# Kernel optimization log

Measured on AMD Instinct MI355X. Metric: run time of the kernel, lower is better.

The kernel has to match this reference:

```python
import jax, jax.numpy as jnp
import numpy as np

BQ, BK = 128, 64  # SpargeAttn-style Q/K block sizes
NEG = -1e30


def _block_mask(q, k, simthreshd1, cdfthreshd, scale):
    """Mean-similarity block selection: a (q-block, k-block) pair is pruned only
    when both blocks are self-similar (mean cosine sim to block mean exceeds the
    per-head simthreshd1) AND it is not in the top-CDF mass (cdfthreshd) of the
    compressed block-level softmax."""
    B, H, L, D = q.shape
    nq, nk = L // BQ, L // BK
    qb = q.reshape(B, H, nq, BQ, D)
    kb = k.reshape(B, H, nk, BK, D)
    qm = qb.mean(3)  # [B,H,nq,D] block means
    km = kb.mean(3)  # [B,H,nk,D]

    def blocksim(xb, xm):
        xn = xb / (jnp.linalg.norm(xb, axis=-1, keepdims=True) + 1e-6)
        mn = xm / (jnp.linalg.norm(xm, axis=-1, keepdims=True) + 1e-6)
        return jnp.einsum('bhntd,bhnd->bhnt', xn, mn).mean(-1)  # [B,H,n]

    th = simthreshd1[None, :, None]
    comp_q = blocksim(qb, qm) > th  # [B,H,nq] self-similar q blocks
    comp_k = blocksim(kb, km) > th  # [B,H,nk]

    # compressed attention over block means, then CDF-based top-mass selection
    p = jax.nn.softmax(jnp.einsum('bhqd,bhkd->bhqk', qm, km) * scale, axis=-1)
    order = jnp.argsort(-p, axis=-1)
    sp = jnp.take_along_axis(p, order, axis=-1)
    csum = jnp.cumsum(sp, axis=-1)
    keep_sorted = (csum - sp) < cdfthreshd[None, :, None, None]  # prefix covering tau
    rank = jnp.argsort(order, axis=-1)  # inverse permutation
    selected = jnp.take_along_axis(keep_sorted, rank, axis=-1)  # [B,H,nq,nk]

    return selected | ~(comp_q[..., :, None] & comp_k[..., None, :])


def setup_inputs() -> dict:
    key = jax.random.key(0)
    kq, kk, kv, kc = jax.random.split(key, 4)
    B, H, L, D = 1, 16, 2048, 64
    return {
        'q': jax.random.normal(kq, (B, H, L, D), dtype=jnp.float32),
        'k': jax.random.normal(kk, (B, H, L, D), dtype=jnp.float32),
        'v': jax.random.normal(kv, (B, H, L, D), dtype=jnp.float32),
        'simthreshd1': jnp.zeros((H,), dtype=jnp.float32),
        'cdfthreshd': jax.random.uniform(kc, (H,), dtype=jnp.float32),
    }


def reference(q, k, v, simthreshd1, cdfthreshd):
    B, H, L, D = q.shape
    scale = 1.0 / np.sqrt(D).astype(np.float32)
    # smooth_k: subtract per-(B,H) key mean (softmax-invariant shift, matches kernel)
    k = k - k.mean(axis=-2, keepdims=True)
    bmask = _block_mask(q, k, simthreshd1, cdfthreshd, scale)  # [B,H,nq,nk] bool
    mask_tok = jnp.repeat(jnp.repeat(bmask, BQ, axis=2), BK, axis=3)  # [B,H,L,L]
    s = jnp.einsum('bhqd,bhkd->bhqk', q, k) * scale
    s = jnp.where(mask_tok, s, NEG)
    p = jax.nn.softmax(s, axis=-1)
    return jnp.einsum('bhqk,bhkd->bhqd', p, v)
```

## Files before the change

### kernel.cpp

```cpp
#include <hip/hip_runtime.h>

#define HH 16
#define LL 2048
#define DD 64
#define BQ 128
#define BK 64
#define NQ (LL/BQ)
#define NK (LL/BK)
#define SCALE 0.125f
#define QSCALE (0.125f * 1.44269504f)

typedef __attribute__((ext_vector_type(8))) short s8v;
typedef __attribute__((ext_vector_type(4))) float f4v;

static __device__ __forceinline__ ushort f2bf(float x) {
    unsigned u = __float_as_uint(x);
    u += 0x7fff + ((u >> 16) & 1);
    return (ushort)(u >> 16);
}

__global__ void kmean1_kernel(const float* __restrict__ k, float* __restrict__ kpart) {
    int b = blockIdx.x;
    int h = blockIdx.y;
    int t = threadIdx.x;
    int d = t & 63, c = t >> 6;
    const float* kh = k + ((size_t)h*LL + (size_t)b*256) * DD;
    float s = 0.f;
    for (int l = c*64; l < c*64 + 64; ++l) s += kh[(size_t)l * DD + d];
    __shared__ float red[4][64];
    red[c][d] = s;
    __syncthreads();
    if (t < 64) kpart[((size_t)h*8 + b)*64 + t] = red[0][t]+red[1][t]+red[2][t]+red[3][t];
}

__global__ __launch_bounds__(128) void stats_kernel(
        const float* __restrict__ q, const float* __restrict__ k, const float* __restrict__ v,
        const float* __restrict__ kpart, const float* __restrict__ simth,
        float* __restrict__ qm, float* __restrict__ km,
        int* __restrict__ compq, int* __restrict__ compk,
        ushort* __restrict__ qb, ushort* __restrict__ kb, ushort* __restrict__ vTb) {
    __shared__ __align__(16) char smem[34304];
    int h = blockIdx.y, t = threadIdx.x;

    if ((int)blockIdx.x < NQ) {
        int qi = blockIdx.x;
        float (*xs)[DD+1] = (float(*)[DD+1])smem;
        float* mean = (float*)(smem + 33280);
        float* red  = (float*)(smem + 33536);
        size_t row = (size_t)h*LL + (size_t)qi*BQ + t;
        const float* rp = q + row * DD;
        float x[DD]; float n2 = 0.f;
        #pragma unroll
        for (int d = 0; d < DD; d += 4) {
            float4 v4 = *(const float4*)(rp + d);
            x[d]=v4.x; x[d+1]=v4.y; x[d+2]=v4.z; x[d+3]=v4.w;
            n2 += v4.x*v4.x + v4.y*v4.y + v4.z*v4.z + v4.w*v4.w;
        }
        #pragma unroll
        for (int d = 0; d < DD; d += 4) {
            ushort4 o;
            o.x = f2bf(x[d]*QSCALE);   o.y = f2bf(x[d+1]*QSCALE);
            o.z = f2bf(x[d+2]*QSCALE); o.w = f2bf(x[d+3]*QSCALE);
            *(ushort4*)(qb + row*DD + d) = o;
        }
        #pragma unroll
        for (int d = 0; d < DD; ++d) xs[t][d] = x[d];
        __syncthreads();
        {
            int d = t & 63, hf = t >> 6;
            float s = 0.f;
            for (int r = hf*64; r < hf*64 + 64; ++r) s += xs[r][d];
            red[t] = s;
        }
        __syncthreads();
        if (t < DD) mean[t] = (red[t] + red[64 + t]) * (1.0f/BQ);
        __syncthreads();
        float dot = 0.f, m2 = 0.f;
        #pragma unroll
        for (int d = 0; d < DD; ++d) { dot += x[d]*mean[d]; m2 += mean[d]*mean[d]; }
        float cs = dot / ((sqrtf(n2) + 1e-6f) * (sqrtf(m2) + 1e-6f));
        __syncthreads();
        red[t] = cs; __syncthreads();
        for (int sft = BQ/2; sft > 0; sft >>= 1) {
            if (t < sft) red[t] += red[t + sft];
            __syncthreads();
        }
        if (t == 0) compq[h*NQ + qi] = (red[0] * (1.0f/BQ)) > simth[h] ? 1 : 0;
        if (t < DD) qm[((size_t)h*NQ + qi)*DD + t] = mean[t];
    } else {
        int ki = blockIdx.x - NQ;
        float* mu_s = (float*)smem;
        float (*xs)[DD+1] = (float(*)[DD+1])(smem + 256);
        ushort (*vs)[66]  = (ushort(*)[66])(smem + 256 + 16640);
        float* mean = (float*)(smem + 256 + 16640 + 8448);
        float* red  = (float*)(smem + 256 + 16640 + 8448 + 256);
        if (t < 64) {
            float s = 0.f;
            #pragma unroll
            for (int b = 0; b < 8; ++b) s += kpart[((size_t)h*8 + b)*64 + t];
            mu_s[t] = s * (1.0f/LL);
        }
        __syncthreads();
        size_t rowb = (size_t)h*LL + (size_t)ki*BK;
        float x[DD]; float n2 = 0.f;
        if (t < 64) {
            const float* rp = k + (rowb + t) * DD;
            #pragma unroll
            for (int d = 0; d < DD; d += 4) {
                float4 v4 = *(const float4*)(rp + d);
                v4.x -= mu_s[d]; v4.y -= mu_s[d+1]; v4.z -= mu_s[d+2]; v4.w -= mu_s[d+3];
                x[d]=v4.x; x[d+1]=v4.y; x[d+2]=v4.z; x[d+3]=v4.w;
                n2 += v4.x*v4.x + v4.y*v4.y + v4.z*v4.z + v4.w*v4.w;
            }
            #pragma unroll
            for (int d = 0; d < DD; d += 4) {
                ushort4 o;
                o.x = f2bf(x[d]);   o.y = f2bf(x[d+1]);
                o.z = f2bf(x[d+2]); o.w = f2bf(x[d+3]);
                *(ushort4*)(kb + (rowb + t)*DD + d) = o;
            }
            #pragma unroll
            for (int d = 0; d < DD; ++d) xs[t][d] = x[d];
        } else {
            int tk = t - 64;
            const float* vp = v + (rowb + tk) * DD;
            #pragma unroll
            for (int d = 0; d < DD; d += 4) {
                float4 v4 = *(const float4*)(vp + d);
                vs[tk][d]   = f2bf(v4.x); vs[tk][d+1] = f2bf(v4.y);
                vs[tk][d+2] = f2bf(v4.z); vs[tk][d+3] = f2bf(v4.w);
            }
        }
        __syncthreads();
        if (t < 64) {
            size_t vbase = ((size_t)h*DD + t)*LL + (size_t)ki*64;
            #pragma unroll
            for (int r8 = 0; r8 < 64; r8 += 8) {
                s8v o;
                #pragma unroll
                for (int e = 0; e < 8; ++e) o[e] = (short)vs[r8+e][t];
                *(s8v*)(vTb + vbase + r8) = o;
            }
            float s = 0.f;
            for (int r = 0; r < BK; ++r) s += xs[r][t];
            mean[t] = s * (1.0f/BK);
        }
        __syncthreads();
        if (t < 64) {
            float dot = 0.f, m2 = 0.f;
            #pragma unroll
            for (int d = 0; d < DD; ++d) { dot += x[d]*mean[d]; m2 += mean[d]*mean[d]; }
            float cs = dot / ((sqrtf(n2) + 1e-6f) * (sqrtf(m2) + 1e-6f));
            red[t] = cs;
        }
        __syncthreads();
        for (int sft = 32; sft > 0; sft >>= 1) {
            if (t < sft) red[t] += red[t + sft];
            __syncthreads();
        }
        if (t == 0) compk[h*NK + ki] = (red[0] * (1.0f/BK)) > simth[h] ? 1 : 0;
        if (t < 64) km[((size_t)h*NK + ki)*DD + t] = mean[t];
    }
}

__global__ __launch_bounds__(256, 2) void attn_kernel(
        const ushort* __restrict__ qb, const ushort* __restrict__ kb,
        const ushort* __restrict__ vTb,
        const float* __restrict__ qm, const float* __restrict__ km,
        const int* __restrict__ compq, const int* __restrict__ compk,
        const float* __restrict__ cdfth, float* __restrict__ out) {
    __shared__ __align__(16) char shmem[69632];
    ushort* pl = (ushort*)shmem + (threadIdx.x >> 6) * 64 * 72;
    float*  Ob = (float*)shmem;
    float*  mb = (float*)(shmem + 67584);
    float*  lb = (float*)(shmem + 68608);

    int bid  = blockIdx.x;
    int slot = bid >> 3;
    int h    = ((slot >> 5) << 3) | (bid & 7);
    int qi   = (slot & 31) >> 1;
    int half = slot & 1;
    int tid  = threadIdx.x;
    int w    = tid >> 6;
    int l    = tid & 63;
    int lo = l & 15, hi = l >> 4;
    int r0 = qi*BQ + half*64;

    unsigned msk;
    {
        int j = l & 31;
        const float* qv = qm + ((size_t)h*NQ + qi)*DD;
        const float* kv = km + ((size_t)h*NK + j)*DD;
        float s = 0.f;
        #pragma unroll
        for (int d = 0; d < DD; d += 4) {
            float4 a = *(const float4*)(qv + d);
            float4 b = *(const float4*)(kv + d);
            s += a.x*b.x; s += a.y*b.y; s += a.z*b.z; s += a.w*b.w;
        }
        s *= SCALE;
        float mx = s;
        #pragma unroll
        for (int xm = 1; xm <= 16; xm <<= 1) mx = fmaxf(mx, __shfl_xor(mx, xm, 32));
        float e = expf(s - mx);
        float den = 0.f;
        for (int i = 0; i < 32; ++i) den += __shfl(e, i, 32);
        float p = e / den;
        float mass = 0.f;
        for (int i = 0; i < 32; ++i) {
            float pi = __shfl(p, i, 32);
            if (pi > p || (pi == p && i < j)) mass += pi;
        }
        int keep = (mass < cdfth[h]) || !(compq[h*NQ+qi] && compk[h*NK+j]);
        unsigned long long bal = __ballot(keep != 0);
        msk = (unsigned)bal;
    }

    const ushort* qh = qb  + (size_t)h*LL*DD;
    const ushort* kh = kb  + (size_t)h*LL*DD;
    const ushort* vh = vTb + (size_t)h*DD*LL;

    s8v qf[4][2];
    #pragma unroll
    for (int qt = 0; qt < 4; ++qt)
        #pragma unroll
        for (int kk = 0; kk < 2; ++kk)
            qf[qt][kk] = *(const s8v*)(qh + (size_t)(r0 + qt*16 + lo)*DD + kk*32 + hi*8);

    f4v O[4][4];
    float m[4], lsum[4];
    #pragma unroll
    for (int qt = 0; qt < 4; ++qt) {
        m[qt] = -1e30f; lsum[qt] = 0.f;
        #pragma unroll
        for (int dt = 0; dt < 4; ++dt) O[qt][dt] = (f4v){0.f,0.f,0.f,0.f};
    }

    unsigned mm = msk; int rank = 0;
    while (mm) {
        int j = __ffs(mm) - 1; mm &= mm - 1;
        if (((rank++) & 3) != w) continue;

        const ushort* kbj = kh + (size_t)j*BK*DD;
        const ushort* vbj = vh + (size_t)j*BK;

        s8v kf[4][2];
        #pragma unroll
        for (int kt = 0; kt < 4; ++kt)
            #pragma unroll
            for (int kk = 0; kk < 2; ++kk)
                kf[kt][kk] = *(const s8v*)(kbj + (size_t)(kt*16 + lo)*DD + kk*32 + hi*8);

        f4v S[4][4];
        #pragma unroll
        for (int kt = 0; kt < 4; ++kt)
            #pragma unroll
            for (int qt = 0; qt < 4; ++qt)
                S[kt][qt] = (f4v){0.f,0.f,0.f,0.f};
        __builtin_amdgcn_s_setprio(1);
        #pragma unroll
        for (int kk = 0; kk < 2; ++kk)
            #pragma unroll
            for (int kt = 0; kt < 4; ++kt)
                #pragma unroll
                for (int qt = 0; qt < 4; ++qt)
                    S[kt][qt] = __builtin_amdgcn_mfma_f32_16x16x32_bf16(kf[kt][kk], qf[qt][kk], S[kt][qt], 0, 0, 0);
        __builtin_amdgcn_s_setprio(0);

        s8v vf[2][4];
        #pragma unroll
        for (int kk = 0; kk < 2; ++kk)
            #pragma unroll
            for (int dt = 0; dt < 4; ++dt)
                vf[kk][dt] = *(const s8v*)(vbj + (size_t)(dt*16 + lo)*LL + kk*32 + hi*8);

        float pm[4];
        #pragma unroll
        for (int qt = 0; qt < 4; ++qt) {
            float a0 = fmaxf(fmaxf(S[0][qt][0],S[0][qt][1]), fmaxf(S[0][qt][2],S[0][qt][3]));
            float a1 = fmaxf(fmaxf(S[1][qt][0],S[1][qt][1]), fmaxf(S[1][qt][2],S[1][qt][3]));
            float a2 = fmaxf(fmaxf(S[2][qt][0],S[2][qt][1]), fmaxf(S[2][qt][2],S[2][qt][3]));
            float a3 = fmaxf(fmaxf(S[3][qt][0],S[3][qt][1]), fmaxf(S[3][qt][2],S[3][qt][3]));
            float p = fmaxf(fmaxf(a0,a1), fmaxf(a2,a3));
            p = fmaxf(p, __shfl_xor(p, 16));
            p = fmaxf(p, __shfl_xor(p, 32));
            pm[qt] = p;
        }
        bool grow = (pm[0] > m[0]+8.0f) | (pm[1] > m[1]+8.0f) |
                    (pm[2] > m[2]+8.0f) | (pm[3] > m[3]+8.0f);
        if (__any(grow)) {
            float alpha[4];
            #pragma unroll
            for (int qt = 0; qt < 4; ++qt) {
                float mn = fmaxf(m[qt], pm[qt]);
                alpha[qt] = __builtin_amdgcn_exp2f(m[qt] - mn);
                lsum[qt] *= alpha[qt];
                m[qt] = mn;
            }
            #pragma unroll
            for (int qt = 0; qt < 4; ++qt)
                #pragma unroll
                for (int r = 0; r < 4; ++r) {
                    float a = __shfl(alpha[qt], hi*4 + r);
                    #pragma unroll
                    for (int dt = 0; dt < 4; ++dt) O[qt][dt][r] *= a;
                }
        }
        #pragma unroll
        for (int qt = 0; qt < 4; ++qt) {
            float ps = 0.f;
            #pragma unroll
            for (int kt = 0; kt < 4; ++kt) {
                float p0 = __builtin_amdgcn_exp2f(S[kt][qt][0] - m[qt]);
                float p1 = __builtin_amdgcn_exp2f(S[kt][qt][1] - m[qt]);
                float p2 = __builtin_amdgcn_exp2f(S[kt][qt][2] - m[qt]);
                float p3 = __builtin_amdgcn_exp2f(S[kt][qt][3] - m[qt]);
                ps += (p0 + p1) + (p2 + p3);
                unsigned c01, c23;
                asm("v_cvt_pk_bf16_f32 %0, %1, %2" : "=v"(c01) : "v"(p0), "v"(p1));
                asm("v_cvt_pk_bf16_f32 %0, %1, %2" : "=v"(c23) : "v"(p2), "v"(p3));
                *(uint2*)&pl[(qt*16 + lo)*72 + kt*16 + hi*4] = make_uint2(c01, c23);
            }
            lsum[qt] += ps;
        }
        __builtin_amdgcn_s_setprio(1);
        #pragma unroll
        for (int qt = 0; qt < 4; ++qt)
            #pragma unroll
            for (int kk = 0; kk < 2; ++kk) {
                s8v pa = *(const s8v*)&pl[(qt*16 + lo)*72 + kk*32 + hi*8];
                #pragma unroll
                for (int dt = 0; dt < 4; ++dt)
                    O[qt][dt] = __builtin_amdgcn_mfma_f32_16x16x32_bf16(pa, vf[kk][dt], O[qt][dt], 0, 0, 0);
            }
        __builtin_amdgcn_s_setprio(0);
    }

    #pragma unroll
    for (int qt = 0; qt < 4; ++qt) {
        lsum[qt] += __shfl_xor(lsum[qt], 16);
        lsum[qt] += __shfl_xor(lsum[qt], 32);
    }

    __syncthreads();

    if (hi == 0) {
        #pragma unroll
        for (int qt = 0; qt < 4; ++qt) {
            mb[w*64 + qt*16 + lo] = m[qt];
            lb[w*64 + qt*16 + lo] = lsum[qt];
        }
    }
    #pragma unroll
    for (int qt = 0; qt < 4; ++qt)
        #pragma unroll
        for (int dt = 0; dt < 4; ++dt)
            #pragma unroll
            for (int r = 0; r < 4; ++r)
                Ob[w*4224 + (qt*16 + hi*4 + r)*66 + dt*16 + lo] = O[qt][dt][r];
    __syncthreads();

    {
        int q = l;
        float mw0 = mb[q], mw1 = mb[64+q], mw2 = mb[128+q], mw3 = mb[192+q];
        float ms = fmaxf(fmaxf(mw0,mw1), fmaxf(mw2,mw3));
        float c0 = __builtin_amdgcn_exp2f(mw0 - ms);
        float c1 = __builtin_amdgcn_exp2f(mw1 - ms);
        float c2 = __builtin_amdgcn_exp2f(mw2 - ms);
        float c3 = __builtin_amdgcn_exp2f(mw3 - ms);
        float ls = lb[q]*c0 + lb[64+q]*c1 + lb[128+q]*c2 + lb[192+q]*c3;
        float inv = 1.0f / ls;
        float* orow = out + ((size_t)h*LL + r0 + q)*DD + w*16;
        #pragma unroll
        for (int i4 = 0; i4 < 4; ++i4) {
            float4 o;
            #pragma unroll
            for (int e = 0; e < 4; ++e) {
                int d = w*16 + i4*4 + e;
                float acc = Ob[q*66 + d]*c0 + Ob[4224 + q*66 + d]*c1
                          + Ob[8448 + q*66 + d]*c2 + Ob[12672 + q*66 + d]*c3;
                ((float*)&o)[e] = acc * inv;
            }
            *(float4*)(orow + i4*4) = o;
        }
    }
}

extern "C" void kernel_launch(void* const* d_in, const int* in_sizes, int n_in,
                              void* d_out, int out_size, void* d_ws, size_t ws_size,
                              hipStream_t stream) {
    const float* q     = (const float*)d_in[0];
    const float* k     = (const float*)d_in[1];
    const float* v     = (const float*)d_in[2];
    const float* simth = (const float*)d_in[3];
    const float* cdfth = (const float*)d_in[4];
    float* out = (float*)d_out;

    float* ws    = (float*)d_ws;
    float* kpart = ws;
    float* qm    = kpart + HH*8*64;
    float* km    = qm + HH*NQ*DD;
    int*   compq = (int*)(km + HH*NK*DD);
    int*   compk = compq + HH*NQ;
    size_t off = (size_t)((char*)(compk + HH*NK) - (char*)d_ws);
    off = (off + 15) & ~(size_t)15;
    ushort* qbuf = (ushort*)((char*)d_ws + off);
    ushort* kbuf = qbuf + (size_t)HH*LL*DD;
    ushort* vTb  = kbuf + (size_t)HH*LL*DD;

    kmean1_kernel<<<dim3(8, HH), 256, 0, stream>>>(k, kpart);
    stats_kernel<<<dim3(NQ + NK, HH), 128, 0, stream>>>(q, k, v, kpart, simth,
                                                        qm, km, compq, compk,
                                                        qbuf, kbuf, vTb);
    attn_kernel<<<dim3(NQ*2*HH), 256, 0, stream>>>(qbuf, kbuf, vTb,
                                                   qm, km, compq, compk, cdfth, out);
}
```

Before: 72.99 us.

## Split query tile into quarters and software-pipeline QK with softmax/PV

Each attention block now handles 32 query rows instead of 64, doubling the grid and shrinking shared memory and register accumulators. The key-block loop is restructured into a two-stage ping-pong: the next block's K load and QK MFMA are issued while the current block's softmax and PV run, using double-buffered P tiles in LDS. This aims to raise occupancy and hide load and softmax latency behind matrix work. In exchange, each block recomputes the block mask and reloads K/V for fewer query rows, which raises total K/V traffic.

```diff
diff --git a/kernel.cpp b/kernel.cpp
--- a/kernel.cpp
+++ b/kernel.cpp
@@ -169,22 +169,24 @@
         const float* __restrict__ qm, const float* __restrict__ km,
         const int* __restrict__ compq, const int* __restrict__ compk,
         const float* __restrict__ cdfth, float* __restrict__ out) {
-    __shared__ __align__(16) char shmem[69632];
-    ushort* pl = (ushort*)shmem + (threadIdx.x >> 6) * 64 * 72;
+    __shared__ __align__(16) char shmem[37888];
+    int tid  = threadIdx.x;
+    int w    = tid >> 6;
+    ushort* plA = (ushort*)shmem + w * 2304;
+    ushort* plB = (ushort*)shmem + 9216 + w * 2304;
     float*  Ob = (float*)shmem;
-    float*  mb = (float*)(shmem + 67584);
-    float*  lb = (float*)(shmem + 68608);
+    float*  mb = (float*)(shmem + 36864);
+    float*  lb = (float*)(shmem + 37376);
 
     int bid  = blockIdx.x;
     int slot = bid >> 3;
-    int h    = ((slot >> 5) << 3) | (bid & 7);
-    int qi   = (slot & 31) >> 1;
-    int half = slot & 1;
-    int tid  = threadIdx.x;
-    int w    = tid >> 6;
+    int h    = ((slot >> 6) << 3) | (bid & 7);
+    int rem  = slot & 63;
+    int qi   = rem >> 2;
+    int quarter = rem & 3;
     int l    = tid & 63;
     int lo = l & 15, hi = l >> 4;
-    int r0 = qi*BQ + half*64;
+    int r0 = qi*BQ + quarter*32;
 
     unsigned msk;
     {
@@ -220,42 +222,51 @@
     const ushort* kh = kb  + (size_t)h*LL*DD;
     const ushort* vh = vTb + (size_t)h*DD*LL;
 
-    s8v qf[4][2];
+    s8v qf[2][2];
     #pragma unroll
-    for (int qt = 0; qt < 4; ++qt)
+    for (int qt = 0; qt < 2; ++qt)
         #pragma unroll
         for (int kk = 0; kk < 2; ++kk)
             qf[qt][kk] = *(const s8v*)(qh + (size_t)(r0 + qt*16 + lo)*DD + kk*32 + hi*8);
 
-    f4v O[4][4];
-    float m[4], lsum[4];
+    f4v O[2][4];
+    float m[2], lsum[2];
     #pragma unroll
-    for (int qt = 0; qt < 4; ++qt) {
+    for (int qt = 0; qt < 2; ++qt) {
         m[qt] = -1e30f; lsum[qt] = 0.f;
         #pragma unroll
         for (int dt = 0; dt < 4; ++dt) O[qt][dt] = (f4v){0.f,0.f,0.f,0.f};
     }
 
     unsigned mm = msk; int rank = 0;
-    while (mm) {
-        int j = __ffs(mm) - 1; mm &= mm - 1;
-        if (((rank++) & 3) != w) continue;
-
+    auto nextj = [&]() -> int {
+        while (mm) {
+            int j = __ffs(mm) - 1; mm &= mm - 1;
+            if (((rank++) & 3) == w) return j;
+        }
+        return -1;
+    };
+    auto loadK = [&](s8v (&kf)[4][2], int j) {
         const ushort* kbj = kh + (size_t)j*BK*DD;
-        const ushort* vbj = vh + (size_t)j*BK;
-
-        s8v kf[4][2];
         #pragma unroll
         for (int kt = 0; kt < 4; ++kt)
             #pragma unroll
             for (int kk = 0; kk < 2; ++kk)
                 kf[kt][kk] = *(const s8v*)(kbj + (size_t)(kt*16 + lo)*DD + kk*32 + hi*8);
-
-        f4v S[4][4];
+    };
+    auto loadV = [&](s8v (&vf)[2][4], int j) {
+        const ushort* vbj = vh + (size_t)j*BK;
+        #pragma unroll
+        for (int kk = 0; kk < 2; ++kk)
+            #pragma unroll
+            for (int dt = 0; dt < 4; ++dt)
+                vf[kk][dt] = *(const s8v*)(vbj + (size_t)(dt*16 + lo)*LL + kk*32 + hi*8);
+    };
+    auto doQK = [&](f4v (&S)[4][2], const s8v (&kf)[4][2]) {
         #pragma unroll
         for (int kt = 0; kt < 4; ++kt)
             #pragma unroll
-            for (int qt = 0; qt < 4; ++qt)
+            for (int qt = 0; qt < 2; ++qt)
                 S[kt][qt] = (f4v){0.f,0.f,0.f,0.f};
         __builtin_amdgcn_s_setprio(1);
         #pragma unroll
@@ -263,20 +274,14 @@
             #pragma unroll
             for (int kt = 0; kt < 4; ++kt)
                 #pragma unroll
-                for (int qt = 0; qt < 4; ++qt)
+                for (int qt = 0; qt < 2; ++qt)
                     S[kt][qt] = __builtin_amdgcn_mfma_f32_16x16x32_bf16(kf[kt][kk], qf[qt][kk], S[kt][qt], 0, 0, 0);
         __builtin_amdgcn_s_setprio(0);
-
-        s8v vf[2][4];
-        #pragma unroll
-        for (int kk = 0; kk < 2; ++kk)
-            #pragma unroll
-            for (int dt = 0; dt < 4; ++dt)
-                vf[kk][dt] = *(const s8v*)(vbj + (size_t)(dt*16 + lo)*LL + kk*32 + hi*8);
-
-        float pm[4];
-        #pragma unroll
-        for (int qt = 0; qt < 4; ++qt) {
+    };
+    auto softmaxPack = [&](f4v (&S)[4][2], ushort* pp) {
+        float pm2[2];
+        #pragma unroll
+        for (int qt = 0; qt < 2; ++qt) {
             float a0 = fmaxf(fmaxf(S[0][qt][0],S[0][qt][1]), fmaxf(S[0][qt][2],S[0][qt][3]));
             float a1 = fmaxf(fmaxf(S[1][qt][0],S[1][qt][1]), fmaxf(S[1][qt][2],S[1][qt][3]));
             float a2 = fmaxf(fmaxf(S[2][qt][0],S[2][qt][1]), fmaxf(S[2][qt][2],S[2][qt][3]));
@@ -284,21 +289,20 @@
             float p = fmaxf(fmaxf(a0,a1), fmaxf(a2,a3));
             p = fmaxf(p, __shfl_xor(p, 16));
             p = fmaxf(p, __shfl_xor(p, 32));
-            pm[qt] = p;
-        }
-        bool grow = (pm[0] > m[0]+8.0f) | (pm[1] > m[1]+8.0f) |
-                    (pm[2] > m[2]+8.0f) | (pm[3] > m[3]+8.0f);
+            pm2[qt] = p;
+        }
+        bool grow = (pm2[0] > m[0]+8.0f) | (pm2[1] > m[1]+8.0f);
         if (__any(grow)) {
-            float alpha[4];
-            #pragma unroll
-            for (int qt = 0; qt < 4; ++qt) {
-                float mn = fmaxf(m[qt], pm[qt]);
+            float alpha[2];
+            #pragma unroll
+            for (int qt = 0; qt < 2; ++qt) {
+                float mn = fmaxf(m[qt], pm2[qt]);
                 alpha[qt] = __builtin_amdgcn_exp2f(m[qt] - mn);
                 lsum[qt] *= alpha[qt];
                 m[qt] = mn;
             }
             #pragma unroll
-            for (int qt = 0; qt < 4; ++qt)
+            for (int qt = 0; qt < 2; ++qt)
                 #pragma unroll
                 for (int r = 0; r < 4; ++r) {
                     float a = __shfl(alpha[qt], hi*4 + r);
@@ -307,7 +311,7 @@
                 }
         }
         #pragma unroll
-        for (int qt = 0; qt < 4; ++qt) {
+        for (int qt = 0; qt < 2; ++qt) {
             float ps = 0.f;
             #pragma unroll
             for (int kt = 0; kt < 4; ++kt) {
@@ -319,25 +323,53 @@
                 unsigned c01, c23;
                 asm("v_cvt_pk_bf16_f32 %0, %1, %2" : "=v"(c01) : "v"(p0), "v"(p1));
                 asm("v_cvt_pk_bf16_f32 %0, %1, %2" : "=v"(c23) : "v"(p2), "v"(p3));
-                *(uint2*)&pl[(qt*16 + lo)*72 + kt*16 + hi*4] = make_uint2(c01, c23);
+                *(uint2*)&pp[(qt*16 + lo)*72 + kt*16 + hi*4] = make_uint2(c01, c23);
             }
             lsum[qt] += ps;
         }
+    };
+    auto doPV = [&](const s8v (&vf)[2][4], const ushort* pp) {
         __builtin_amdgcn_s_setprio(1);
         #pragma unroll
-        for (int qt = 0; qt < 4; ++qt)
+        for (int qt = 0; qt < 2; ++qt)
             #pragma unroll
             for (int kk = 0; kk < 2; ++kk) {
-                s8v pa = *(const s8v*)&pl[(qt*16 + lo)*72 + kk*32 + hi*8];
+                s8v pa = *(const s8v*)&pp[(qt*16 + lo)*72 + kk*32 + hi*8];
                 #pragma unroll
                 for (int dt = 0; dt < 4; ++dt)
                     O[qt][dt] = __builtin_amdgcn_mfma_f32_16x16x32_bf16(pa, vf[kk][dt], O[qt][dt], 0, 0, 0);
             }
         __builtin_amdgcn_s_setprio(0);
+    };
+
+    s8v kfA[4][2], kfB[4][2], vf[2][4];
+    f4v SA[4][2], SB[4][2];
+    int jcur = nextj();
+    if (jcur >= 0) {
+        loadK(kfA, jcur);
+        doQK(SA, kfA);
+        for (;;) {
+            int jn = nextj();
+            if (jn >= 0) loadK(kfB, jn);
+            loadV(vf, jcur);
+            softmaxPack(SA, plA);
+            if (jn >= 0) doQK(SB, kfB);
+            doPV(vf, plA);
+            if (jn < 0) break;
+            jcur = jn;
+            jn = nextj();
+            if (jn >= 0) loadK(kfA, jn);
+            loadV(vf, jcur);
+            softmaxPack(SB, plB);
+            if (jn >= 0) doQK(SA, kfA);
+            doPV(vf, plB);
+            if (jn < 0) break;
+            jcur = jn;
+        }
     }
 
     #pragma unroll
-    for (int qt = 0; qt < 4; ++qt) {
+    for (int qt = 0; qt < 2; ++qt) {
         lsum[qt] += __shfl_xor(lsum[qt], 16);
         lsum[qt] += __shfl_xor(lsum[qt], 32);
     }
@@ -346,39 +378,39 @@
 
     if (hi == 0) {
         #pragma unroll
-        for (int qt = 0; qt < 4; ++qt) {
-            mb[w*64 + qt*16 + lo] = m[qt];
-            lb[w*64 + qt*16 + lo] = lsum[qt];
+        for (int qt = 0; qt < 2; ++qt) {
+            mb[w*32 + qt*16 + lo] = m[qt];
+            lb[w*32 + qt*16 + lo] = lsum[qt];
         }
     }
     #pragma unroll
-    for (int qt = 0; qt < 4; ++qt)
+    for (int qt = 0; qt < 2; ++qt)
         #pragma unroll
         for (int dt = 0; dt < 4; ++dt)
             #pragma unroll
             for (int r = 0; r < 4; ++r)
-                Ob[w*4224 + (qt*16 + hi*4 + r)*66 + dt*16 + lo] = O[qt][dt][r];
+                Ob[w*2112 + (qt*16 + hi*4 + r)*66 + dt*16 + lo] = O[qt][dt][r];
     __syncthreads();
 
     {
-        int q = l;
-        float mw0 = mb[q], mw1 = mb[64+q], mw2 = mb[128+q], mw3 = mb[192+q];
+        int q = tid & 31, c = tid >> 5, d0 = c*8;
+        float mw0 = mb[q], mw1 = mb[32+q], mw2 = mb[64+q], mw3 = mb[96+q];
         float ms = fmaxf(fmaxf(mw0,mw1), fmaxf(mw2,mw3));
         float c0 = __builtin_amdgcn_exp2f(mw0 - ms);
         float c1 = __builtin_amdgcn_exp2f(mw1 - ms);
         float c2 = __builtin_amdgcn_exp2f(mw2 - ms);
         float c3 = __builtin_amdgcn_exp2f(mw3 - ms);
-        float ls = lb[q]*c0 + lb[64+q]*c1 + lb[128+q]*c2 + lb[192+q]*c3;
+        float ls = lb[q]*c0 + lb[32+q]*c1 + lb[64+q]*c2 + lb[96+q]*c3;
         float inv = 1.0f / ls;
-        float* orow = out + ((size_t)h*LL + r0 + q)*DD + w*16;
-        #pragma unroll
-        for (int i4 = 0; i4 < 4; ++i4) {
+        float* orow = out + ((size_t)h*LL + r0 + q)*DD + d0;
+        #pragma unroll
+        for (int i4 = 0; i4 < 2; ++i4) {
             float4 o;
             #pragma unroll
             for (int e = 0; e < 4; ++e) {
-                int d = w*16 + i4*4 + e;
-                float acc = Ob[q*66 + d]*c0 + Ob[4224 + q*66 + d]*c1
-                          + Ob[8448 + q*66 + d]*c2 + Ob[12672 + q*66 + d]*c3;
+                int d = d0 + i4*4 + e;
+                float acc = Ob[q*66 + d]*c0 + Ob[2112 + q*66 + d]*c1
+                          + Ob[4224 + q*66 + d]*c2 + Ob[6336 + q*66 + d]*c3;
                 ((float*)&o)[e] = acc * inv;
             }
             *(float4*)(orow + i4*4) = o;
@@ -412,6 +444,6 @@
     stats_kernel<<<dim3(NQ + NK, HH), 128, 0, stream>>>(q, k, v, kpart, simth,
                                                         qm, km, compq, compk,
                                                         qbuf, kbuf, vTb);
-    attn_kernel<<<dim3(NQ*2*HH), 256, 0, stream>>>(qbuf, kbuf, vTb,
+    attn_kernel<<<dim3(NQ*4*HH), 256, 0, stream>>>(qbuf, kbuf, vTb,
                                                    qm, km, compq, compk, cdfth, out);
 }
```

Result: slower. 126.2 us (+72.9%).
